# Optimization experiments

Hardware: AMD Instinct MI355X
Metric: run time of the kernel (lower is better)

## Reference

```python
import jax, jax.numpy as jnp
import numpy as np

N_HEAD = 16
ROPE_BASE = 10000.0

def rotate_half(x):
    half = x.shape[-1] // 2
    return jnp.concatenate((-x[..., half:], x[..., :half]), axis=-1)

def rope_freqs(T, head_dim, dtype):
    inv_freq = 1.0 / (ROPE_BASE ** (jnp.arange(0, head_dim, 2, dtype=jnp.float32) / head_dim))
    t = jnp.arange(T, dtype=jnp.float32)
    freqs = t[:, None] * inv_freq[None, :]          # [T, head_dim//2]
    emb = jnp.concatenate((freqs, freqs), axis=-1)  # [T, head_dim]
    return emb.astype(dtype)

def setup_inputs() -> dict:
    key = jax.random.key(0)
    ks = jax.random.split(key, 9)
    B, T, C = 2, 2048, 1024
    s = 1.0 / np.sqrt(C)
    return {
        'x':  jax.random.normal(ks[0], (B, T, C), jnp.float32),
        'Wq': jax.random.normal(ks[1], (C, C), jnp.float32) * s,
        'bq': jnp.zeros((C,), jnp.float32),
        'Wk': jax.random.normal(ks[2], (C, C), jnp.float32) * s,
        'bk': jnp.zeros((C,), jnp.float32),
        'Wv': jax.random.normal(ks[3], (C, C), jnp.float32) * s,
        'bv': jnp.zeros((C,), jnp.float32),
        'Wp': jax.random.normal(ks[4], (C, C), jnp.float32) * s,
        'bp': jnp.zeros((C,), jnp.float32),
    }

def reference(x, Wq, bq, Wk, bk, Wv, bv, Wp, bp):
    B, T, C = x.shape
    H = N_HEAD
    D = C // H
    # torch Linear: y = x @ W.T + b
    def heads(y):
        return y.reshape(B, T, H, D).transpose(0, 2, 1, 3)  # [B,H,T,D]
    q = heads(x @ Wq.T + bq)
    k = heads(x @ Wk.T + bk)
    v = heads(x @ Wv.T + bv)
    # inline RoPE
    emb = rope_freqs(T, D, x.dtype)          # [T, D]
    cos, sin = jnp.cos(emb), jnp.sin(emb)
    q = q * cos + rotate_half(q) * sin
    k = k * cos + rotate_half(k) * sin
    # full T x T scores with causal masked softmax
    att = jnp.einsum('bhtd,bhsd->bhts', q, k) * (1.0 / jnp.sqrt(jnp.array(D, x.dtype)))
    causal = jnp.tril(jnp.ones((T, T), bool))
    att = jnp.where(causal[None, None], att, jnp.array(-jnp.inf, att.dtype))
    att = jax.nn.softmax(att, axis=-1)
    y = jnp.einsum('bhts,bhsd->bhtd', att, v)  # [B,H,T,D]
    y = y.transpose(0, 2, 1, 3).reshape(B, T, C)
    return y @ Wp.T + bp
```

## Files before the change

kernel.cpp:

```cpp
#include <hip/hip_runtime.h>
#include <hip/hip_bf16.h>
#include <stdint.h>

typedef unsigned short u16;
typedef __attribute__((ext_vector_type(8))) short bf16x8;
typedef __attribute__((ext_vector_type(4))) float f32x4;

typedef const __attribute__((address_space(1))) unsigned int* gu32p;
typedef __attribute__((address_space(3))) unsigned int* lu32p;

__device__ __forceinline__ void gl_lds16(const u16* g, u16* l) {
  __builtin_amdgcn_global_load_lds((gu32p)(const void*)g, (lu32p)(void*)l, 16, 0, 0);
}

__device__ __forceinline__ u16 f2bf(float f) {
  union { float f; unsigned u; } v; v.f = f;
  unsigned r = v.u + 0x7fffu + ((v.u >> 16) & 1u);
  return (u16)(r >> 16);
}
__device__ __forceinline__ void st2bf(u16* p0, u16* p1, float a, float b) {
  union { __hip_bfloat162 h; u16 u[2]; } cv;
  cv.h = __float22bfloat162_rn(make_float2(a, b));
  *p0 = cv.u[0]; *p1 = cv.u[1];
}

__global__ void convert_kernel(const float4* __restrict__ x, const float4* __restrict__ wq,
                               const float4* __restrict__ wk, const float4* __restrict__ wv,
                               const float4* __restrict__ wp,
                               u16* __restrict__ xb, u16* __restrict__ wqb, u16* __restrict__ wkb,
                               u16* __restrict__ wvb, u16* __restrict__ wpb,
                               float2* __restrict__ tab) {
  int i = blockIdx.x * 256 + threadIdx.x;
  const int NX = 1048576, NW = 262144, NCONV = NX + 4 * NW;
  if (i >= NCONV) {
    int j = i - NCONV;
    int d = j & 31, t = j >> 5;
    float ang = (float)t * expf(-0.28782313662425572f * (float)d);
    tab[j] = make_float2(cosf(ang), sinf(ang));
    return;
  }
  const float4* src; u16* dst; int off;
  if (i < NX)            { src = x;  dst = xb;  off = i; }
  else if (i < NX + NW)  { src = wq; dst = wqb; off = i - NX; }
  else if (i < NX + 2*NW){ src = wk; dst = wkb; off = i - NX - NW; }
  else if (i < NX + 3*NW){ src = wv; dst = wvb; off = i - NX - 2*NW; }
  else                   { src = wp; dst = wpb; off = i - NX - 3*NW; }
  float4 v = src[off];
  ushort4 ov = make_ushort4(f2bf(v.x), f2bf(v.y), f2bf(v.z), f2bf(v.w));
  *(ushort4*)&dst[off * 4] = ov;
}

template<int FUSE_ROPE, int OUT_BF16, int TRANS_V>
__global__ __launch_bounds__(256) void gemm_bt_kernel(
    const u16* __restrict__ A,
    const u16* __restrict__ B0, const u16* __restrict__ B1, const u16* __restrict__ B2,
    const float* __restrict__ bias0, const float* __restrict__ bias1, const float* __restrict__ bias2,
    void* out0, void* out1, void* out2, const float2* __restrict__ tab)
{
  __shared__ __align__(16) u16 As[2][4096];
  __shared__ __align__(16) u16 Bs[2][4096];
  const int z = blockIdx.z;
  const u16* Bw = (z == 0) ? B0 : (z == 1) ? B1 : B2;
  const float* bias = (z == 0) ? bias0 : (z == 1) ? bias1 : bias2;
  void* outv = (z == 0) ? out0 : (z == 1) ? out1 : out2;
  const int tid = threadIdx.x, lane = tid & 63, w = tid >> 6;
  const int wr = w >> 1, wc = w & 1;
  const int quad = lane >> 4, l15 = lane & 15;
  const int m0 = blockIdx.y * 128, n0 = blockIdx.x * 128;
  const int sr = lane >> 2, sc = (lane & 3) * 8;

  auto stg = [&](int kt, int bf) {
    const int k0 = kt * 32;
    #pragma unroll
    for (int p = 0; p < 2; p++) {
      gl_lds16(A  + (m0 + p*64 + w*16 + sr) * 1024 + k0 + sc, &As[bf][p*2048 + w*512]);
      gl_lds16(Bw + (n0 + p*64 + w*16 + sr) * 1024 + k0 + sc, &Bs[bf][p*2048 + w*512]);
    }
  };

  f32x4 acc[4][4] = {};
  stg(0, 0);
  for (int kt = 0; kt < 32; kt++) {
    __syncthreads();
    if (kt < 31) stg(kt + 1, (kt + 1) & 1);
    const int bf = kt & 1;
    bf16x8 af[4], bfr[4];
    #pragma unroll
    for (int mt = 0; mt < 4; mt++)
      af[mt] = *(const bf16x8*)&As[bf][(wr*64 + mt*16 + l15) * 32 + quad*8];
    #pragma unroll
    for (int nt = 0; nt < 4; nt++)
      bfr[nt] = *(const bf16x8*)&Bs[bf][(wc*64 + nt*16 + l15) * 32 + quad*8];
    #pragma unroll
    for (int mt = 0; mt < 4; mt++)
      #pragma unroll
      for (int nt = 0; nt < 4; nt++)
        acc[mt][nt] = __builtin_amdgcn_mfma_f32_16x16x32_bf16(af[mt], bfr[nt], acc[mt][nt], 0, 0, 0);
  }

  if (TRANS_V && z == 2) {
    const int bb = m0 >> 11, tg0 = (m0 & 2047) + wr*64 + quad*4;
    #pragma unroll
    for (int nt = 0; nt < 4; nt++) {
      const int c = n0 + wc*64 + nt*16 + l15;
      const float bv = bias[c];
      u16* vrow = (u16*)outv + (size_t)(bb*1024 + c) * 2048 + tg0;
      #pragma unroll
      for (int mt = 0; mt < 4; mt++) {
        ushort4 pk;
        pk.x = f2bf(acc[mt][nt][0] + bv); pk.y = f2bf(acc[mt][nt][1] + bv);
        pk.z = f2bf(acc[mt][nt][2] + bv); pk.w = f2bf(acc[mt][nt][3] + bv);
        *(ushort4*)&vrow[mt*16] = pk;
      }
    }
    return;
  }

  #pragma unroll
  for (int mt = 0; mt < 4; mt++) {
    #pragma unroll
    for (int r = 0; r < 4; r++) {
      const int row = m0 + wr*64 + mt*16 + quad*4 + r;
      float v[4];
      #pragma unroll
      for (int nt = 0; nt < 4; nt++)
        v[nt] = acc[mt][nt][r] + bias[n0 + wc*64 + nt*16 + l15];
      if (FUSE_ROPE && z < 2) {
        const int t = row & 2047;
        #pragma unroll
        for (int nt = 0; nt < 2; nt++) {
          const int d = nt*16 + l15;
          float2 cs = tab[t*32 + d];
          float x0 = v[nt], x1 = v[nt+2];
          v[nt]   = x0 * cs.x - x1 * cs.y;
          v[nt+2] = x1 * cs.x + x0 * cs.y;
        }
      }
      #pragma unroll
      for (int nt = 0; nt < 4; nt++) {
        const int col = n0 + wc*64 + nt*16 + l15;
        if (OUT_BF16) ((u16*)outv)[row * 1024 + col] = f2bf(v[nt]);
        else          ((float*)outv)[row * 1024 + col] = v[nt];
      }
    }
  }
}

__global__ __launch_bounds__(512) void attn_kernel(
    const u16* __restrict__ qg, const u16* __restrict__ kg,
    const u16* __restrict__ vtg, u16* __restrict__ yg)
{
  __shared__ __align__(16) u16 K_lds[2][128 * 64];
  __shared__ __align__(16) u16 V_lds[2][64 * 128];
  __shared__ __align__(16) u16 P_lds[8][2][16 * 128];
  const int x = blockIdx.x;
  const int hh = blockIdx.y, b = blockIdx.z;
  const int tid = threadIdx.x, lane = tid & 63, w = tid >> 6;
  const int wt = w >> 2;
  const int quad = lane >> 4, l15 = lane & 15;
  const int bh = b * (2048 * 1024) + hh * 64;
  const int vtb = (b * 16 + hh) * 131072;

  const int qtA = x, qtB = 15 - x;
  const int qt_w = wt ? qtB : qtA;
  const int wl = w & 3;

  bf16x8 qf[2][2];
  #pragma unroll
  for (int rg = 0; rg < 2; rg++) {
    const int qrow = qt_w*128 + rg*64 + wl*16 + l15;
    qf[rg][0] = *(const bf16x8*)&qg[bh + qrow*1024 + quad*8];
    qf[rg][1] = *(const bf16x8*)&qg[bh + qrow*1024 + 32 + quad*8];
  }
  f32x4 o[2][4] = {};
  f32x4 l5[2] = {};

  bf16x8 ones;
  #pragma unroll
  for (int i2 = 0; i2 < 8; i2++) ones[i2] = (short)0x3F80;

  const float c = 0.18033688011112042f;

  auto do_stage = [&](int j, int bf) {
    #pragma unroll
    for (int p = 0; p < 2; p++) {
      const int seg = w*2 + p;
      const int r = seg*8 + (lane >> 3);
      const int g = (lane & 7) ^ (r & 7);
      gl_lds16(kg + bh + (j*128 + r) * 1024 + g*8, &K_lds[bf][seg*512]);
    }
    #pragma unroll
    for (int p = 0; p < 2; p++) {
      const int seg = w*2 + p;
      const int r = seg*4 + (lane >> 4);
      const int g = (lane & 15) ^ (r & 15);
      gl_lds16(vtg + vtb + r * 2048 + j*128 + g*8, &V_lds[bf][seg*512]);
    }
  };

  do_stage(0, 0);
  for (int j = 0; j <= qtB; j++) {
    __syncthreads();
    if (j < qtB) do_stage(j + 1, (j + 1) & 1);
    const int bf = j & 1;
    if (wt == 0 && j > qtA) continue;
    const bool diag = (j == qt_w);

    f32x4 s[2][8];
    #pragma unroll
    for (int nt = 0; nt < 8; nt++) {
      const int krow = (nt*16 + l15) * 64;
      const int g0 = ((quad)     ^ (l15 & 7)) * 8;
      const int g1 = ((4 + quad) ^ (l15 & 7)) * 8;
      bf16x8 kf0 = *(const bf16x8*)&K_lds[bf][krow + g0];
      bf16x8 kf1 = *(const bf16x8*)&K_lds[bf][krow + g1];
      #pragma unroll
      for (int rg = 0; rg < 2; rg++) {
        f32x4 z = {};
        z = __builtin_amdgcn_mfma_f32_16x16x32_bf16(qf[rg][0], kf0, z, 0, 0, 0);
        z = __builtin_amdgcn_mfma_f32_16x16x32_bf16(qf[rg][1], kf1, z, 0, 0, 0);
        s[rg][nt] = z;
      }
    }
    if (diag) {
      #pragma unroll
      for (int rg = 0; rg < 2; rg++) {
        const int trow = rg*64 + wl*16 + quad*4;
        #pragma unroll
        for (int nt = 0; nt < 8; nt++)
          #pragma unroll
          for (int r = 0; r < 4; r++)
            if (nt*16 + l15 > trow + r) s[rg][nt][r] = -1e30f;
      }
    }
    #pragma unroll
    for (int rg = 0; rg < 2; rg++)
      #pragma unroll
      for (int r = 0; r < 4; r++) {
        const int R = quad*4 + r;
        u16* pp = &P_lds[w][rg][R*128 + (l15 & 7)];
        #pragma unroll
        for (int nt = 0; nt < 8; nt += 2) {
          float p0 = exp2f(s[rg][nt][r] * c);
          float p1 = exp2f(s[rg][nt+1][r] * c);
          const int g0 = ((nt*2     + (l15 >> 3)) ^ (R & 7)) * 8;
          const int g1 = (((nt+1)*2 + (l15 >> 3)) ^ (R & 7)) * 8;
          st2bf(pp + g0, pp + g1, p0, p1);
        }
      }
    #pragma unroll
    for (int ss = 0; ss < 4; ss++) {
      const int pg = ((ss*4 + quad) ^ (l15 & 7)) * 8;
      bf16x8 pf0 = *(const bf16x8*)&P_lds[w][0][l15*128 + pg];
      bf16x8 pf1 = *(const bf16x8*)&P_lds[w][1][l15*128 + pg];
      l5[0] = __builtin_amdgcn_mfma_f32_16x16x32_bf16(pf0, ones, l5[0], 0, 0, 0);
      l5[1] = __builtin_amdgcn_mfma_f32_16x16x32_bf16(pf1, ones, l5[1], 0, 0, 0);
      #pragma unroll
      for (int dt = 0; dt < 4; dt++) {
        const int vg = ((ss*4 + quad) ^ l15) * 8;
        bf16x8 vf = *(const bf16x8*)&V_lds[bf][(dt*16 + l15)*128 + vg];
        o[0][dt] = __builtin_amdgcn_mfma_f32_16x16x32_bf16(pf0, vf, o[0][dt], 0, 0, 0);
        o[1][dt] = __builtin_amdgcn_mfma_f32_16x16x32_bf16(pf1, vf, o[1][dt], 0, 0, 0);
      }
    }
  }

  #pragma unroll
  for (int rg = 0; rg < 2; rg++)
    #pragma unroll
    for (int r = 0; r < 4; r++) {
      float inv = 1.0f / l5[rg][r];
      u16* yr = &yg[bh + (qt_w*128 + rg*64 + wl*16 + quad*4 + r) * 1024 + l15];
      st2bf(yr,      yr + 16, o[rg][0][r] * inv, o[rg][1][r] * inv);
      st2bf(yr + 32, yr + 48, o[rg][2][r] * inv, o[rg][3][r] * inv);
    }
}

extern "C" void kernel_launch(void* const* d_in, const int* in_sizes, int n_in,
                              void* d_out, int out_size, void* d_ws, size_t ws_size,
                              hipStream_t stream) {
  const float* x  = (const float*)d_in[0];
  const float* Wq = (const float*)d_in[1];
  const float* bq = (const float*)d_in[2];
  const float* Wk = (const float*)d_in[3];
  const float* bk = (const float*)d_in[4];
  const float* Wv = (const float*)d_in[5];
  const float* bv = (const float*)d_in[6];
  const float* Wp = (const float*)d_in[7];
  const float* bp = (const float*)d_in[8];

  char* ws = (char*)d_ws;
  u16* xb  = (u16*)(ws);
  u16* wqb = (u16*)(ws + (8u  << 20));
  u16* wkb = (u16*)(ws + (10u << 20));
  u16* wvb = (u16*)(ws + (12u << 20));
  u16* wpb = (u16*)(ws + (14u << 20));
  u16* qb  = (u16*)(ws + (16u << 20));
  u16* kb  = (u16*)(ws + (24u << 20));
  u16* vtb = (u16*)(ws + (32u << 20));
  float2* tab = (float2*)(ws + (40u << 20));
  u16* yb = xb;

  convert_kernel<<<8448, 256, 0, stream>>>((const float4*)x, (const float4*)Wq, (const float4*)Wk,
                                           (const float4*)Wv, (const float4*)Wp,
                                           xb, wqb, wkb, wvb, wpb, tab);
  gemm_bt_kernel<1, 1, 1><<<dim3(8, 32, 3), 256, 0, stream>>>(xb, wqb, wkb, wvb, bq, bk, bv,
                                                              (void*)qb, (void*)kb, (void*)vtb, tab);
  attn_kernel<<<dim3(8, 16, 2), 512, 0, stream>>>(qb, kb, vtb, yb);
  gemm_bt_kernel<0, 0, 0><<<dim3(8, 32, 1), 256, 0, stream>>>(yb, wpb, wpb, wpb, bp, bp, bp,
                                                              (void*)d_out, (void*)d_out, (void*)d_out, tab);
}
```

Measured before the change: 209.7 us.

## Give each wave rows from both paired query tiles to balance causal work

Each attention block pairs a short query tile (qtA) with a long one (qtB). Previously half the waves owned qtA and went idle once past its diagonal, while the other half processed the remaining key tiles. Now every wave owns 16 rows of qtA and 16 rows of qtB, so all eight waves stay active for every key tile, with the qtA work gated by a wave-uniform branch. This is meant to even out per-wave work and shorten the critical path. It adds branching inside the inner loop, and the gain may be limited if waves sharing a SIMD were already balanced in aggregate.

Result: no change. 213.0 us (+1.6%).

```diff
diff --git a/kernel.cpp b/kernel.cpp
--- a/kernel.cpp
+++ b/kernel.cpp
@@ -156,24 +156,24 @@
   const int x = blockIdx.x;
   const int hh = blockIdx.y, b = blockIdx.z;
   const int tid = threadIdx.x, lane = tid & 63, w = tid >> 6;
-  const int wt = w >> 2;
   const int quad = lane >> 4, l15 = lane & 15;
   const int bh = b * (2048 * 1024) + hh * 64;
   const int vtb = (b * 16 + hh) * 131072;
 
   const int qtA = x, qtB = 15 - x;
-  const int qt_w = wt ? qtB : qtA;
-  const int wl = w & 3;
-
-  bf16x8 qf[2][2];
-  #pragma unroll
-  for (int rg = 0; rg < 2; rg++) {
-    const int qrow = qt_w*128 + rg*64 + wl*16 + l15;
-    qf[rg][0] = *(const bf16x8*)&qg[bh + qrow*1024 + quad*8];
-    qf[rg][1] = *(const bf16x8*)&qg[bh + qrow*1024 + 32 + quad*8];
-  }
-  f32x4 o[2][4] = {};
-  f32x4 l5[2] = {};
+  const int wrow = w*16;
+
+  bf16x8 qfA[2], qfB[2];
+  {
+    const int rA = qtA*128 + wrow + l15;
+    const int rB = qtB*128 + wrow + l15;
+    qfA[0] = *(const bf16x8*)&qg[bh + rA*1024 + quad*8];
+    qfA[1] = *(const bf16x8*)&qg[bh + rA*1024 + 32 + quad*8];
+    qfB[0] = *(const bf16x8*)&qg[bh + rB*1024 + quad*8];
+    qfB[1] = *(const bf16x8*)&qg[bh + rB*1024 + 32 + quad*8];
+  }
+  f32x4 oA[4] = {}, oB[4] = {};
+  f32x4 l5A = {}, l5B = {};
 
   bf16x8 ones;
   #pragma unroll
@@ -203,10 +203,9 @@
     __syncthreads();
     if (j < qtB) do_stage(j + 1, (j + 1) & 1);
     const int bf = j & 1;
-    if (wt == 0 && j > qtA) continue;
-    const bool diag = (j == qt_w);
-
-    f32x4 s[2][8];
+    const bool doA = (j <= qtA);
+
+    f32x4 sA[8], sB[8];
     #pragma unroll
     for (int nt = 0; nt < 8; nt++) {
       const int krow = (nt*16 + l15) * 64;
@@ -214,66 +213,90 @@
       const int g1 = ((4 + quad) ^ (l15 & 7)) * 8;
       bf16x8 kf0 = *(const bf16x8*)&K_lds[bf][krow + g0];
       bf16x8 kf1 = *(const bf16x8*)&K_lds[bf][krow + g1];
-      #pragma unroll
-      for (int rg = 0; rg < 2; rg++) {
-        f32x4 z = {};
-        z = __builtin_amdgcn_mfma_f32_16x16x32_bf16(qf[rg][0], kf0, z, 0, 0, 0);
-        z = __builtin_amdgcn_mfma_f32_16x16x32_bf16(qf[rg][1], kf1, z, 0, 0, 0);
-        s[rg][nt] = z;
-      }
-    }
-    if (diag) {
-      #pragma unroll
-      for (int rg = 0; rg < 2; rg++) {
-        const int trow = rg*64 + wl*16 + quad*4;
+      f32x4 z = {};
+      z = __builtin_amdgcn_mfma_f32_16x16x32_bf16(qfB[0], kf0, z, 0, 0, 0);
+      z = __builtin_amdgcn_mfma_f32_16x16x32_bf16(qfB[1], kf1, z, 0, 0, 0);
+      sB[nt] = z;
+      if (doA) {
+        f32x4 za = {};
+        za = __builtin_amdgcn_mfma_f32_16x16x32_bf16(qfA[0], kf0, za, 0, 0, 0);
+        za = __builtin_amdgcn_mfma_f32_16x16x32_bf16(qfA[1], kf1, za, 0, 0, 0);
+        sA[nt] = za;
+      }
+    }
+    const int trow = wrow + quad*4;
+    if (j == qtB) {
+      #pragma unroll
+      for (int nt = 0; nt < 8; nt++)
         #pragma unroll
-        for (int nt = 0; nt < 8; nt++)
-          #pragma unroll
-          for (int r = 0; r < 4; r++)
-            if (nt*16 + l15 > trow + r) s[rg][nt][r] = -1e30f;
-      }
-    }
-    #pragma unroll
-    for (int rg = 0; rg < 2; rg++)
+        for (int r = 0; r < 4; r++)
+          if (nt*16 + l15 > trow + r) sB[nt][r] = -1e30f;
+    }
+    if (doA && j == qtA) {
+      #pragma unroll
+      for (int nt = 0; nt < 8; nt++)
+        #pragma unroll
+        for (int r = 0; r < 4; r++)
+          if (nt*16 + l15 > trow + r) sA[nt][r] = -1e30f;
+    }
+    #pragma unroll
+    for (int r = 0; r < 4; r++) {
+      const int R = quad*4 + r;
+      u16* ppB = &P_lds[w][1][R*128 + (l15 & 7)];
+      #pragma unroll
+      for (int nt = 0; nt < 8; nt += 2) {
+        float p0 = exp2f(sB[nt][r] * c);
+        float p1 = exp2f(sB[nt+1][r] * c);
+        const int g0 = ((nt*2     + (l15 >> 3)) ^ (R & 7)) * 8;
+        const int g1 = (((nt+1)*2 + (l15 >> 3)) ^ (R & 7)) * 8;
+        st2bf(ppB + g0, ppB + g1, p0, p1);
+      }
+    }
+    if (doA) {
       #pragma unroll
       for (int r = 0; r < 4; r++) {
         const int R = quad*4 + r;
-        u16* pp = &P_lds[w][rg][R*128 + (l15 & 7)];
+        u16* ppA = &P_lds[w][0][R*128 + (l15 & 7)];
         #pragma unroll
         for (int nt = 0; nt < 8; nt += 2) {
-          float p0 = exp2f(s[rg][nt][r] * c);
-          float p1 = exp2f(s[rg][nt+1][r] * c);
+          float p0 = exp2f(sA[nt][r] * c);
+          float p1 = exp2f(sA[nt+1][r] * c);
           const int g0 = ((nt*2     + (l15 >> 3)) ^ (R & 7)) * 8;
           const int g1 = (((nt+1)*2 + (l15 >> 3)) ^ (R & 7)) * 8;
-          st2bf(pp + g0, pp + g1, p0, p1);
+          st2bf(ppA + g0, ppA + g1, p0, p1);
         }
       }
+    }
     #pragma unroll
     for (int ss = 0; ss < 4; ss++) {
       const int pg = ((ss*4 + quad) ^ (l15 & 7)) * 8;
-      bf16x8 pf0 = *(const bf16x8*)&P_lds[w][0][l15*128 + pg];
-      bf16x8 pf1 = *(const bf16x8*)&P_lds[w][1][l15*128 + pg];
-      l5[0] = __builtin_amdgcn_mfma_f32_16x16x32_bf16(pf0, ones, l5[0], 0, 0, 0);
-      l5[1] = __builtin_amdgcn_mfma_f32_16x16x32_bf16(pf1, ones, l5[1], 0, 0, 0);
+      bf16x8 pfB = *(const bf16x8*)&P_lds[w][1][l15*128 + pg];
+      l5B = __builtin_amdgcn_mfma_f32_16x16x32_bf16(pfB, ones, l5B, 0, 0, 0);
+      bf16x8 pfA = {};
+      if (doA) {
+        pfA = *(const bf16x8*)&P_lds[w][0][l15*128 + pg];
+        l5A = __builtin_amdgcn_mfma_f32_16x16x32_bf16(pfA, ones, l5A, 0, 0, 0);
+      }
       #pragma unroll
       for (int dt = 0; dt < 4; dt++) {
         const int vg = ((ss*4 + quad) ^ l15) * 8;
         bf16x8 vf = *(const bf16x8*)&V_lds[bf][(dt*16 + l15)*128 + vg];
-        o[0][dt] = __builtin_amdgcn_mfma_f32_16x16x32_bf16(pf0, vf, o[0][dt], 0, 0, 0);
-        o[1][dt] = __builtin_amdgcn_mfma_f32_16x16x32_bf16(pf1, vf, o[1][dt], 0, 0, 0);
+        oB[dt] = __builtin_amdgcn_mfma_f32_16x16x32_bf16(pfB, vf, oB[dt], 0, 0, 0);
+        if (doA) oA[dt] = __builtin_amdgcn_mfma_f32_16x16x32_bf16(pfA, vf, oA[dt], 0, 0, 0);
       }
     }
   }
 
   #pragma unroll
-  for (int rg = 0; rg < 2; rg++)
-    #pragma unroll
-    for (int r = 0; r < 4; r++) {
-      float inv = 1.0f / l5[rg][r];
-      u16* yr = &yg[bh + (qt_w*128 + rg*64 + wl*16 + quad*4 + r) * 1024 + l15];
-      st2bf(yr,      yr + 16, o[rg][0][r] * inv, o[rg][1][r] * inv);
-      st2bf(yr + 32, yr + 48, o[rg][2][r] * inv, o[rg][3][r] * inv);
-    }
+  for (int r = 0; r < 4; r++) {
+    float ia = 1.0f / l5A[r], ib = 1.0f / l5B[r];
+    u16* yA = &yg[bh + (qtA*128 + wrow + quad*4 + r) * 1024 + l15];
+    u16* yB = &yg[bh + (qtB*128 + wrow + quad*4 + r) * 1024 + l15];
+    st2bf(yA,      yA + 16, oA[0][r] * ia, oA[1][r] * ia);
+    st2bf(yA + 32, yA + 48, oA[2][r] * ia, oA[3][r] * ia);
+    st2bf(yB,      yB + 16, oB[0][r] * ib, oB[1][r] * ib);
+    st2bf(yB + 32, yB + 48, oB[2][r] * ib, oB[3][r] * ib);
+  }
 }
 
 extern "C" void kernel_launch(void* const* d_in, const int* in_sizes, int n_in,
```
